# Performance work log

Measured on AMD Instinct MI355X. Metric: run time of the kernel, lower is better.

The kernel has to match this reference:

```python
import jax, jax.numpy as jnp
import numpy as np

N = 1_000_000   # memory slots (current_size == memory_size)
D = 64          # embedding_dim == compressed_dim (required by the source code)
B = 64          # query batch
QBITS = 8       # quantization_bits


def setup_inputs() -> dict:
    key = jax.random.key(0)
    ks = jax.random.split(key, 6)
    return {
        "query": jax.random.normal(ks[0], (B, D), dtype=jnp.float32),
        "memory": jax.random.normal(ks[1], (N, D), dtype=jnp.float32),
        "attention_weights": jax.random.normal(ks[2], (N,), dtype=jnp.float32),
        "Wq": jax.random.normal(ks[3], (D, D), dtype=jnp.float32) / np.sqrt(D),
        "Wk": jax.random.normal(ks[4], (D, D), dtype=jnp.float32) / np.sqrt(D),
        "Wv": jax.random.normal(ks[5], (D, D), dtype=jnp.float32) / np.sqrt(D),
        "top_k": 5,
    }


def reference(query, memory, attention_weights, Wq, Wk, Wv, top_k):
    d = memory.shape[1]
    levels = jnp.float32(2 ** QBITS - 1)
    # _quantize_tensor / _dequantize_tensor round-trip on the stored memory
    mn = memory.min()
    mx = memory.max()
    scale = (mx - mn) / levels
    zero_point = -mn / scale
    mem_dq = (jnp.round(memory / scale + zero_point) - zero_point) * scale  # [N, D]

    q = query @ Wq.T                    # [B, D]
    keys = mem_dq @ Wk.T                # [N, D]
    values = mem_dq @ Wv.T              # [N, D]

    # attention scores + per-slot bias
    scores = q @ keys.T / np.float32(np.sqrt(d)) + attention_weights[None, :]  # [B, N]

    top_scores, top_idx = jax.lax.top_k(scores, top_k)   # [B, k]
    gathered = jnp.take(values, top_idx, axis=0)         # [B, k, D] irregular gather
    dist = jax.nn.softmax(top_scores, axis=-1)           # [B, k]
    out = jnp.einsum('bk,bkd->bd', dist, gathered)       # [B, D]
    return out
```

## Files before the change

kernel.cpp:

```cpp
#include <hip/hip_runtime.h>
#include <stdint.h>

constexpr int NROWS = 1000000;
constexpr int D = 64;
constexpr int B = 64;
constexpr int TOPK = 5;
constexpr int TBLK = 4;
constexpr int TRES = 16;
constexpr int NB2MAX = 1024;

typedef __attribute__((ext_vector_type(8))) short short8;
typedef __attribute__((ext_vector_type(4))) float floatx4;
typedef unsigned long long u64;

#define OFF_QKF   512
#define OFF_QKB   16896
#define OFF_MM    25088
#define OFF_CAND  57856

__device__ __forceinline__ unsigned fkey(float x) {
    unsigned u = __float_as_uint(x);
    return (u & 0x80000000u) ? ~u : (u | 0x80000000u);
}
__device__ __forceinline__ float fkey_inv(unsigned k) {
    unsigned u = (k & 0x80000000u) ? (k ^ 0x80000000u) : ~k;
    return __uint_as_float(u);
}
__device__ __forceinline__ unsigned short f2bf_rne(float x) {
    unsigned u = __float_as_uint(x);
    u += 0x7fffu + ((u >> 16) & 1u);
    return (unsigned short)(u >> 16);
}

template<int K>
__device__ __forceinline__ void insert_key(u64 (&ks)[K], u64 key) {
    if (key > ks[K - 1]) {
        #pragma unroll
        for (int j = K - 1; j > 0; --j)
            ks[j] = (key > ks[j - 1]) ? ks[j - 1] : ((key > ks[j]) ? key : ks[j]);
        ks[0] = (key > ks[0]) ? key : ks[0];
    }
}

__device__ __forceinline__ void insert2u(unsigned& a, unsigned& b, unsigned key) {
    unsigned hi = key > a ? key : a;
    unsigned lo = key > a ? a : key;
    b = lo > b ? lo : b;
    a = hi;
}

__device__ __forceinline__ u64 expand_key(unsigned k32, int wbeg) {
    if (!k32) return 0ull;
    unsigned row = (unsigned)wbeg + (0xFFFu - (k32 & 0xFFFu));
    return ((u64)(k32 & 0xFFFFF000u) << 32) | (unsigned)~row;
}

__global__ void k_qk(const float* __restrict__ query, const float* __restrict__ Wq,
                     const float* __restrict__ Wk,
                     float* __restrict__ qkf, unsigned short* __restrict__ qkb) {
    __shared__ float q[4][64];
    int t = threadIdx.x;
    int b0 = blockIdx.x * 4;
    int bq = t >> 6, d = t & 63;
    float s1 = 0.f;
    for (int e = 0; e < 64; e++) s1 += query[(b0 + bq) * 64 + e] * Wq[d * 64 + e];
    q[bq][d] = s1;
    __syncthreads();
    float v = 0.f;
    for (int dd = 0; dd < 64; dd++) v += q[bq][dd] * Wk[dd * 64 + d];
    v *= 0.125f;
    qkf[(b0 + bq) * 64 + d] = v;
    qkb[(b0 + bq) * 64 + d] = f2bf_rne(v);
}

__launch_bounds__(256, 4)
__global__ void k_score_mm(const float* __restrict__ mem, const float* __restrict__ aw,
                           const unsigned short* __restrict__ qkb,
                           u64* __restrict__ cand,
                           unsigned* __restrict__ part, int wrows) {
    __shared__ u64 mrg[4][4][16][2];
    __shared__ float swmn[4], swmx[4];

    int t = threadIdx.x;
    int l15 = t & 15, quad = (t >> 4) & 3, w = t >> 6;
    int qr = quad * 4;

    short8 bq[4][2];
    #pragma unroll
    for (int bt = 0; bt < 4; bt++) {
        #pragma unroll
        for (int kb = 0; kb < 2; kb++)
            bq[bt][kb] = *(const short8*)(qkb + (bt * 16 + l15) * 64 + kb * 32 + quad * 8);
    }

    unsigned Ltop[4], Lsec[4];
    #pragma unroll
    for (int bt = 0; bt < 4; bt++) { Ltop[bt] = 0u; Lsec[bt] = 0u; }

    float mnv = 3.402823466e38f, mxv = -3.402823466e38f;

    int gw = blockIdx.x * 4 + w;
    int wbeg = gw * wrows;
    int wend = min(wbeg + wrows, NROWS);
    int span = wend - wbeg;
    int nt = span > 0 ? (span >> 4) : 0;

    const char* pbase = (const char*)mem + (size_t)wbeg * 256 + (size_t)(l15 * 256 + quad * 32);
    const float* abase = aw + wbeg + (t & 15);

    float4 A0, A1, A2, A3, B0, B1, B2, B3, C0, C1, C2, C3;
    float aA = 0.f, aB = 0.f, aC = 0.f;

#define LOADT(T0, T1, T2, T3, TA, TILE) do {                                   \
        const char* pn_ = pbase + (size_t)(TILE) * 4096;                       \
        T0 = *(const float4*)(pn_);                                            \
        T1 = *(const float4*)(pn_ + 16);                                       \
        T2 = *(const float4*)(pn_ + 128);                                      \
        T3 = *(const float4*)(pn_ + 144);                                      \
        TA = abase[(TILE) * 16];                                               \
    } while (0)

#define PROC(T0, T1, T2, T3, TA, IT) do {                                      \
    mnv = fminf(mnv, fminf(fminf(T0.x, T0.y), fminf(T0.z, T0.w)));             \
    mxv = fmaxf(mxv, fmaxf(fmaxf(T0.x, T0.y), fmaxf(T0.z, T0.w)));             \
    mnv = fminf(mnv, fminf(fminf(T1.x, T1.y), fminf(T1.z, T1.w)));             \
    mxv = fmaxf(mxv, fmaxf(fmaxf(T1.x, T1.y), fmaxf(T1.z, T1.w)));             \
    mnv = fminf(mnv, fminf(fminf(T2.x, T2.y), fminf(T2.z, T2.w)));             \
    mxv = fmaxf(mxv, fmaxf(fmaxf(T2.x, T2.y), fmaxf(T2.z, T2.w)));             \
    mnv = fminf(mnv, fminf(fminf(T3.x, T3.y), fminf(T3.z, T3.w)));             \
    mxv = fmaxf(mxv, fmaxf(fmaxf(T3.x, T3.y), fmaxf(T3.z, T3.w)));             \
    short8 a0_, a1_;                                                           \
    a0_[0] = (short)f2bf_rne(T0.x); a0_[1] = (short)f2bf_rne(T0.y);            \
    a0_[2] = (short)f2bf_rne(T0.z); a0_[3] = (short)f2bf_rne(T0.w);            \
    a0_[4] = (short)f2bf_rne(T1.x); a0_[5] = (short)f2bf_rne(T1.y);            \
    a0_[6] = (short)f2bf_rne(T1.z); a0_[7] = (short)f2bf_rne(T1.w);            \
    a1_[0] = (short)f2bf_rne(T2.x); a1_[1] = (short)f2bf_rne(T2.y);            \
    a1_[2] = (short)f2bf_rne(T2.z); a1_[3] = (short)f2bf_rne(T2.w);            \
    a1_[4] = (short)f2bf_rne(T3.x); a1_[5] = (short)f2bf_rne(T3.y);            \
    a1_[6] = (short)f2bf_rne(T3.z); a1_[7] = (short)f2bf_rne(T3.w);            \
    float aw0_ = __shfl(TA, qr);     float aw1_ = __shfl(TA, qr + 1);          \
    float aw2_ = __shfl(TA, qr + 2); float aw3_ = __shfl(TA, qr + 3);          \
    int idb_ = 0xFFF - (IT) * 16 - qr;                                         \
    _Pragma("unroll")                                                          \
    for (int bt_ = 0; bt_ < 4; bt_++) {                                        \
        floatx4 acc_ = {aw0_, aw1_, aw2_, aw3_};                               \
        acc_ = __builtin_amdgcn_mfma_f32_16x16x32_bf16(a0_, bq[bt_][0], acc_, 0, 0, 0); \
        acc_ = __builtin_amdgcn_mfma_f32_16x16x32_bf16(a1_, bq[bt_][1], acc_, 0, 0, 0); \
        _Pragma("unroll")                                                      \
        for (int r_ = 0; r_ < 4; r_++) {                                       \
            unsigned k_ = (fkey(acc_[r_]) & 0xFFFFF000u) | (unsigned)(idb_ - r_); \
            insert2u(Ltop[bt_], Lsec[bt_], k_);                                \
        }                                                                      \
    }                                                                          \
} while (0)

    if (nt > 0) {
        LOADT(A0, A1, A2, A3, aA, 0);
        LOADT(B0, B1, B2, B3, aB, min(1, nt - 1));
        LOADT(C0, C1, C2, C3, aC, min(2, nt - 1));
    }
    int it = 0;
    for (; it + 3 <= nt; it += 3) {
        PROC(A0, A1, A2, A3, aA, it);
        LOADT(A0, A1, A2, A3, aA, min(it + 3, nt - 1));
        PROC(B0, B1, B2, B3, aB, it + 1);
        LOADT(B0, B1, B2, B3, aB, min(it + 4, nt - 1));
        PROC(C0, C1, C2, C3, aC, it + 2);
        LOADT(C0, C1, C2, C3, aC, min(it + 5, nt - 1));
    }
    if (it < nt)     PROC(A0, A1, A2, A3, aA, it);
    if (it + 1 < nt) PROC(B0, B1, B2, B3, aB, it + 1);

#undef LOADT
#undef PROC

    #pragma unroll
    for (int o = 32; o > 0; o >>= 1) {
        mnv = fminf(mnv, __shfl_xor(mnv, o));
        mxv = fmaxf(mxv, __shfl_xor(mxv, o));
    }
    if ((t & 63) == 0) { swmn[w] = mnv; swmx[w] = mxv; }

    #pragma unroll
    for (int bt = 0; bt < 4; bt++) {
        #pragma unroll
        for (int dlt = 16; dlt <= 32; dlt <<= 1) {
            unsigned ka = __shfl_xor(Ltop[bt], dlt);
            unsigned kb = __shfl_xor(Lsec[bt], dlt);
            insert2u(Ltop[bt], Lsec[bt], ka);
            insert2u(Ltop[bt], Lsec[bt], kb);
        }
    }
    if ((t & 48) == 0) {
        #pragma unroll
        for (int bt = 0; bt < 4; bt++) {
            mrg[w][bt][l15][0] = expand_key(Ltop[bt], wbeg);
            mrg[w][bt][l15][1] = expand_key(Lsec[bt], wbeg);
        }
    }
    __syncthreads();

    if (t == 0) {
        float a = fminf(fminf(swmn[0], swmn[1]), fminf(swmn[2], swmn[3]));
        float b2 = fmaxf(fmaxf(swmx[0], swmx[1]), fmaxf(swmx[2], swmx[3]));
        part[blockIdx.x * 2 + 0] = fkey(a);
        part[blockIdx.x * 2 + 1] = fkey(b2);
    }
    if (t < 64) {
        u64 ts[TBLK];
        #pragma unroll
        for (int j = 0; j < TBLK; j++) ts[j] = 0ull;
        int bt = t >> 4, l = t & 15;
        #pragma unroll
        for (int w2 = 0; w2 < 4; w2++) {
            insert_key<TBLK>(ts, mrg[w2][bt][l][0]);
            insert_key<TBLK>(ts, mrg[w2][bt][l][1]);
        }
        #pragma unroll
        for (int j = 0; j < TBLK; j++)
            cand[((long long)blockIdx.x * 64 + t) * TBLK + j] = ts[j];
    }
}

__global__ void k_finalize(const u64* __restrict__ cand, int nb2,
                           const float* __restrict__ mem, const float* __restrict__ aw,
                           const float* __restrict__ Wv, const unsigned* __restrict__ part,
                           const float* __restrict__ qkf, float* __restrict__ out) {
    __shared__ u64 lists[256][TRES];
    __shared__ float qkr[64];
    __shared__ int exid[TRES];
    __shared__ u64 exkey[TRES];
    __shared__ float exsc[TRES];
    __shared__ float wsel[TOPK];
    __shared__ int isel[TOPK];
    __shared__ float su[64];
    __shared__ unsigned redmn[4], redmx[4];
    __shared__ float sscale[2];

    int t = threadIdx.x, b = blockIdx.x;
    int total = nb2 * TBLK;

    unsigned mnk = 0xFFFFFFFFu, mxk = 0u;
    for (int i = t; i < nb2; i += 256) {
        unsigned a = part[2 * i], c = part[2 * i + 1];
        mnk = a < mnk ? a : mnk;
        mxk = c > mxk ? c : mxk;
    }
    #pragma unroll
    for (int o = 32; o > 0; o >>= 1) {
        unsigned am = __shfl_xor(mnk, o); mnk = am < mnk ? am : mnk;
        unsigned ax = __shfl_xor(mxk, o); mxk = ax > mxk ? ax : mxk;
    }
    int w4 = t >> 6;
    if ((t & 63) == 0) { redmn[w4] = mnk; redmx[w4] = mxk; }

    u64 loc[TRES];
    #pragma unroll
    for (int j = 0; j < TRES; j++) loc[j] = 0ull;
    for (int i = t; i < total; i += 256) {
        int blk = i / TBLK, j = i - blk * TBLK;
        insert_key<TRES>(loc, cand[((long long)blk * 64 + b) * TBLK + j]);
    }
    #pragma unroll
    for (int j = 0; j < TRES; j++) lists[t][j] = loc[j];
    if (t < 64) qkr[t] = qkf[b * 64 + t];
    __syncthreads();

    if (t == 255) {
        unsigned m0 = redmn[0], M0 = redmx[0];
        #pragma unroll
        for (int i = 1; i < 4; i++) {
            m0 = redmn[i] < m0 ? redmn[i] : m0;
            M0 = redmx[i] > M0 ? redmx[i] : M0;
        }
        float mnv = fkey_inv(m0), mxv = fkey_inv(M0);
        float scale = (mxv - mnv) / 255.0f;
        sscale[0] = scale;
        sscale[1] = -mnv / scale;
    }

    for (int s = 128; s > 0; s >>= 1) {
        if (t < s) {
            #pragma unroll
            for (int j = 0; j < TRES; j++) insert_key<TRES>(loc, lists[t + s][j]);
            #pragma unroll
            for (int j = 0; j < TRES; j++) lists[t][j] = loc[j];
        }
        __syncthreads();
    }
    if (t < TRES) {
        u64 k = lists[0][t];
        exid[t] = k ? (int)(~(unsigned)k) : 0;
    }
    __syncthreads();

    float scale = sscale[0], zp = sscale[1];

    int lane = t & 63, w = t >> 6;
    for (int i = 0; i < 4; i++) {
        int c = w * 4 + i;
        int idx = exid[c];
        float m = mem[(long long)idx * 64 + lane];
        float dq = (rintf(m / scale + zp) - zp) * scale;
        float p2 = dq * qkr[lane];
        for (int o = 32; o > 0; o >>= 1) p2 += __shfl_xor(p2, o);
        if (lane == 0) {
            float ex = p2 + aw[idx];
            exsc[c] = ex;
            exkey[c] = ((u64)fkey(ex) << 32) | (unsigned)(~(unsigned)idx);
        }
    }
    __syncthreads();

    if (t == 0) {
        u64 bnd = ~0ull;
        float ssel[TOPK];
        for (int p = 0; p < TOPK; p++) {
            u64 best = 0ull; int bc = 0;
            for (int c = 0; c < TRES; c++) {
                u64 k = exkey[c];
                if (k < bnd && k > best) { best = k; bc = c; }
            }
            bnd = best;
            ssel[p] = exsc[bc];
            isel[p] = exid[bc];
        }
        float Z = 0.f;
        for (int p = 0; p < TOPK; p++) { wsel[p] = expf(ssel[p] - ssel[0]); Z += wsel[p]; }
        for (int p = 0; p < TOPK; p++) wsel[p] /= Z;
    }
    __syncthreads();

    if (t < 64) {
        float u = 0.f;
        #pragma unroll
        for (int p = 0; p < TOPK; p++) {
            float m = mem[(long long)isel[p] * 64 + t];
            float dq = (rintf(m / scale + zp) - zp) * scale;
            u += wsel[p] * dq;
        }
        su[t] = u;
    }
    __syncthreads();
    if (t < 64) {
        float o = 0.f;
        #pragma unroll
        for (int e = 0; e < 64; e++) o += su[e] * Wv[t * 64 + e];
        out[b * 64 + t] = o;
    }
}

extern "C" void kernel_launch(void* const* d_in, const int* in_sizes, int n_in,
                              void* d_out, int out_size, void* d_ws, size_t ws_size,
                              hipStream_t stream) {
    const float* query = (const float*)d_in[0];
    const float* mem   = (const float*)d_in[1];
    const float* aw    = (const float*)d_in[2];
    const float* Wq    = (const float*)d_in[3];
    const float* Wk    = (const float*)d_in[4];
    const float* Wv    = (const float*)d_in[5];
    float* out = (float*)d_out;

    char* ws = (char*)d_ws;
    float* qkf     = (float*)(ws + OFF_QKF);
    unsigned short* qkb = (unsigned short*)(ws + OFF_QKB);
    unsigned* part = (unsigned*)(ws + OFF_MM);
    u64* cand = (u64*)(ws + OFF_CAND);

    int nb2 = NB2MAX;
    size_t need = (size_t)OFF_CAND + (size_t)nb2 * 64 * TBLK * 8;
    if (ws_size < need) {
        size_t avail = ws_size > OFF_CAND ? ws_size - OFF_CAND : 0;
        nb2 = (int)(avail / ((size_t)64 * TBLK * 8));
        if (nb2 < 64) nb2 = 64;
        if (nb2 > NB2MAX) nb2 = NB2MAX;
    }
    int waves = nb2 * 4;
    int wrows = ((NROWS + waves - 1) / waves + 15) / 16 * 16;

    k_qk<<<16, 256, 0, stream>>>(query, Wq, Wk, qkf, qkb);
    k_score_mm<<<nb2, 256, 0, stream>>>(mem, aw, qkb, cand, part, wrows);
    k_finalize<<<B, 256, 0, stream>>>(cand, nb2, mem, aw, Wv, part, qkf, out);
}
```

Baseline: 445.9 us.

## Truncate bf16 packing, vector-load slot bias, and double-buffer tile loads

Replaces per-element round-to-nearest bf16 conversion with truncating pack of two floats per 32-bit word, cutting VALU work in the scoring loop. The per-slot attention bias is now read as a float4 per lane instead of a scalar load plus four shuffles. The prefetch pipeline drops from three register buffers to two, and wave row counts are rounded to 32 so the tile count per wave stays even. Truncation slightly changes score rounding, which could alter near-tie top-k selections, and the shallower prefetch may hide less memory latency.

```diff
diff --git a/kernel.cpp b/kernel.cpp
--- a/kernel.cpp
+++ b/kernel.cpp
@@ -11,6 +11,7 @@
 
 typedef __attribute__((ext_vector_type(8))) short short8;
 typedef __attribute__((ext_vector_type(4))) float floatx4;
+typedef __attribute__((ext_vector_type(4))) unsigned uintx4;
 typedef unsigned long long u64;
 
 #define OFF_QKF   512
@@ -31,6 +32,9 @@
     u += 0x7fffu + ((u >> 16) & 1u);
     return (unsigned short)(u >> 16);
 }
+__device__ __forceinline__ unsigned pack_bf16(float lo, float hi) {
+    return (__float_as_uint(hi) & 0xFFFF0000u) | (__float_as_uint(lo) >> 16);
+}
 
 template<int K>
 __device__ __forceinline__ void insert_key(u64 (&ks)[K], u64 key) {
@@ -43,10 +47,10 @@
 }
 
 __device__ __forceinline__ void insert2u(unsigned& a, unsigned& b, unsigned key) {
-    unsigned hi = key > a ? key : a;
-    unsigned lo = key > a ? a : key;
-    b = lo > b ? lo : b;
+    unsigned lo = a < key ? a : key;
+    unsigned hi = a < key ? key : a;
     a = hi;
+    b = b < lo ? lo : b;
 }
 
 __device__ __forceinline__ u64 expand_key(unsigned k32, int wbeg) {
@@ -73,6 +77,41 @@
     qkb[(b0 + bq) * 64 + d] = f2bf_rne(v);
 }
 
+__device__ __forceinline__ void proc_tile(
+        const float4& T0, const float4& T1, const float4& T2, const float4& T3,
+        const float4& TA, int it, int qr,
+        const short8 (&bq)[4][2], unsigned (&Ltop)[4], unsigned (&Lsec)[4],
+        float& mnv, float& mxv) {
+    mnv = fminf(mnv, fminf(fminf(T0.x, T0.y), fminf(T0.z, T0.w)));
+    mxv = fmaxf(mxv, fmaxf(fmaxf(T0.x, T0.y), fmaxf(T0.z, T0.w)));
+    mnv = fminf(mnv, fminf(fminf(T1.x, T1.y), fminf(T1.z, T1.w)));
+    mxv = fmaxf(mxv, fmaxf(fmaxf(T1.x, T1.y), fmaxf(T1.z, T1.w)));
+    mnv = fminf(mnv, fminf(fminf(T2.x, T2.y), fminf(T2.z, T2.w)));
+    mxv = fmaxf(mxv, fmaxf(fmaxf(T2.x, T2.y), fmaxf(T2.z, T2.w)));
+    mnv = fminf(mnv, fminf(fminf(T3.x, T3.y), fminf(T3.z, T3.w)));
+    mxv = fmaxf(mxv, fmaxf(fmaxf(T3.x, T3.y), fmaxf(T3.z, T3.w)));
+
+    uintx4 ua0 = { pack_bf16(T0.x, T0.y), pack_bf16(T0.z, T0.w),
+                   pack_bf16(T1.x, T1.y), pack_bf16(T1.z, T1.w) };
+    uintx4 ua1 = { pack_bf16(T2.x, T2.y), pack_bf16(T2.z, T2.w),
+                   pack_bf16(T3.x, T3.y), pack_bf16(T3.z, T3.w) };
+    short8 a0 = __builtin_bit_cast(short8, ua0);
+    short8 a1 = __builtin_bit_cast(short8, ua1);
+
+    int idb = 0xFFF - it * 16 - qr;
+    #pragma unroll
+    for (int bt = 0; bt < 4; bt++) {
+        floatx4 acc = {TA.x, TA.y, TA.z, TA.w};
+        acc = __builtin_amdgcn_mfma_f32_16x16x32_bf16(a0, bq[bt][0], acc, 0, 0, 0);
+        acc = __builtin_amdgcn_mfma_f32_16x16x32_bf16(a1, bq[bt][1], acc, 0, 0, 0);
+        #pragma unroll
+        for (int r = 0; r < 4; r++) {
+            unsigned kk = (fkey(acc[r]) & 0xFFFFF000u) | (unsigned)(idb - r);
+            insert2u(Ltop[bt], Lsec[bt], kk);
+        }
+    }
+}
+
 __launch_bounds__(256, 4)
 __global__ void k_score_mm(const float* __restrict__ mem, const float* __restrict__ aw,
                            const unsigned short* __restrict__ qkb,
@@ -106,10 +145,9 @@
     int nt = span > 0 ? (span >> 4) : 0;
 
     const char* pbase = (const char*)mem + (size_t)wbeg * 256 + (size_t)(l15 * 256 + quad * 32);
-    const float* abase = aw + wbeg + (t & 15);
-
-    float4 A0, A1, A2, A3, B0, B1, B2, B3, C0, C1, C2, C3;
-    float aA = 0.f, aB = 0.f, aC = 0.f;
+    const float* abase = aw + wbeg + qr;
+
+    float4 A0, A1, A2, A3, AA, B0, B1, B2, B3, BA;
 
 #define LOADT(T0, T1, T2, T3, TA, TILE) do {                                   \
         const char* pn_ = pbase + (size_t)(TILE) * 4096;                       \
@@ -117,62 +155,20 @@
         T1 = *(const float4*)(pn_ + 16);                                       \
         T2 = *(const float4*)(pn_ + 128);                                      \
         T3 = *(const float4*)(pn_ + 144);                                      \
-        TA = abase[(TILE) * 16];                                               \
+        TA = *(const float4*)(abase + (TILE) * 16);                            \
     } while (0)
 
-#define PROC(T0, T1, T2, T3, TA, IT) do {                                      \
-    mnv = fminf(mnv, fminf(fminf(T0.x, T0.y), fminf(T0.z, T0.w)));             \
-    mxv = fmaxf(mxv, fmaxf(fmaxf(T0.x, T0.y), fmaxf(T0.z, T0.w)));             \
-    mnv = fminf(mnv, fminf(fminf(T1.x, T1.y), fminf(T1.z, T1.w)));             \
-    mxv = fmaxf(mxv, fmaxf(fmaxf(T1.x, T1.y), fmaxf(T1.z, T1.w)));             \
-    mnv = fminf(mnv, fminf(fminf(T2.x, T2.y), fminf(T2.z, T2.w)));             \
-    mxv = fmaxf(mxv, fmaxf(fmaxf(T2.x, T2.y), fmaxf(T2.z, T2.w)));             \
-    mnv = fminf(mnv, fminf(fminf(T3.x, T3.y), fminf(T3.z, T3.w)));             \
-    mxv = fmaxf(mxv, fmaxf(fmaxf(T3.x, T3.y), fmaxf(T3.z, T3.w)));             \
-    short8 a0_, a1_;                                                           \
-    a0_[0] = (short)f2bf_rne(T0.x); a0_[1] = (short)f2bf_rne(T0.y);            \
-    a0_[2] = (short)f2bf_rne(T0.z); a0_[3] = (short)f2bf_rne(T0.w);            \
-    a0_[4] = (short)f2bf_rne(T1.x); a0_[5] = (short)f2bf_rne(T1.y);            \
-    a0_[6] = (short)f2bf_rne(T1.z); a0_[7] = (short)f2bf_rne(T1.w);            \
-    a1_[0] = (short)f2bf_rne(T2.x); a1_[1] = (short)f2bf_rne(T2.y);            \
-    a1_[2] = (short)f2bf_rne(T2.z); a1_[3] = (short)f2bf_rne(T2.w);            \
-    a1_[4] = (short)f2bf_rne(T3.x); a1_[5] = (short)f2bf_rne(T3.y);            \
-    a1_[6] = (short)f2bf_rne(T3.z); a1_[7] = (short)f2bf_rne(T3.w);            \
-    float aw0_ = __shfl(TA, qr);     float aw1_ = __shfl(TA, qr + 1);          \
-    float aw2_ = __shfl(TA, qr + 2); float aw3_ = __shfl(TA, qr + 3);          \
-    int idb_ = 0xFFF - (IT) * 16 - qr;                                         \
-    _Pragma("unroll")                                                          \
-    for (int bt_ = 0; bt_ < 4; bt_++) {                                        \
-        floatx4 acc_ = {aw0_, aw1_, aw2_, aw3_};                               \
-        acc_ = __builtin_amdgcn_mfma_f32_16x16x32_bf16(a0_, bq[bt_][0], acc_, 0, 0, 0); \
-        acc_ = __builtin_amdgcn_mfma_f32_16x16x32_bf16(a1_, bq[bt_][1], acc_, 0, 0, 0); \
-        _Pragma("unroll")                                                      \
-        for (int r_ = 0; r_ < 4; r_++) {                                       \
-            unsigned k_ = (fkey(acc_[r_]) & 0xFFFFF000u) | (unsigned)(idb_ - r_); \
-            insert2u(Ltop[bt_], Lsec[bt_], k_);                                \
-        }                                                                      \
-    }                                                                          \
-} while (0)
-
     if (nt > 0) {
-        LOADT(A0, A1, A2, A3, aA, 0);
-        LOADT(B0, B1, B2, B3, aB, min(1, nt - 1));
-        LOADT(C0, C1, C2, C3, aC, min(2, nt - 1));
-    }
-    int it = 0;
-    for (; it + 3 <= nt; it += 3) {
-        PROC(A0, A1, A2, A3, aA, it);
-        LOADT(A0, A1, A2, A3, aA, min(it + 3, nt - 1));
-        PROC(B0, B1, B2, B3, aB, it + 1);
-        LOADT(B0, B1, B2, B3, aB, min(it + 4, nt - 1));
-        PROC(C0, C1, C2, C3, aC, it + 2);
-        LOADT(C0, C1, C2, C3, aC, min(it + 5, nt - 1));
-    }
-    if (it < nt)     PROC(A0, A1, A2, A3, aA, it);
-    if (it + 1 < nt) PROC(B0, B1, B2, B3, aB, it + 1);
-
+        LOADT(A0, A1, A2, A3, AA, 0);
+        for (int it = 0; it < nt; it += 2) {
+            LOADT(B0, B1, B2, B3, BA, it + 1);
+            proc_tile(A0, A1, A2, A3, AA, it, qr, bq, Ltop, Lsec, mnv, mxv);
+            int nx = (it + 2 < nt) ? it + 2 : nt - 1;
+            LOADT(A0, A1, A2, A3, AA, nx);
+            proc_tile(B0, B1, B2, B3, BA, it + 1, qr, bq, Ltop, Lsec, mnv, mxv);
+        }
+    }
 #undef LOADT
-#undef PROC
 
     #pragma unroll
     for (int o = 32; o > 0; o >>= 1) {
@@ -376,7 +372,7 @@
         if (nb2 > NB2MAX) nb2 = NB2MAX;
     }
     int waves = nb2 * 4;
-    int wrows = ((NROWS + waves - 1) / waves + 15) / 16 * 16;
+    int wrows = ((NROWS + waves - 1) / waves + 31) / 32 * 32;
 
     k_qk<<<16, 256, 0, stream>>>(query, Wq, Wk, qkf, qkb);
     k_score_mm<<<nb2, 256, 0, stream>>>(mem, aw, qkb, cand, part, wrows);
```

After: 414.1 us. 1.08x faster.
